# Optimization experiments

Measured on AMD Instinct MI355X. Metric: run time of the kernel, lower is better.

Reference implementation:

```python
import jax, jax.numpy as jnp
import numpy as np

THRESHOLD = 0.5        # correspondence distance threshold (init kwarg)
MAX_ITERS = 50         # fixed iteration count (open3d's max_iteration)
EPS = 1e-6


def setup_inputs() -> dict:
    key = jax.random.key(0)
    k1, k2 = jax.random.split(key)
    B, N, M = 8, 2048, 2048
    source = jax.random.normal(k1, (B, N, 3), dtype=jnp.float32)
    target = jax.random.normal(k2, (B, M, 3), dtype=jnp.float32)
    return {"source": source, "target": target}


def _icp(source, target):
    """Batched point-to-point ICP. source: (B,N,3), target: (B,M,3) -> (B,4,4)."""
    B, N, _ = source.shape
    dt = source.dtype
    t_sq = jnp.sum(target * target, axis=-1)  # (B,M), constant across iterations

    def step(T, _):
        R, tr = T[:, :3, :3], T[:, :3, 3]
        src = jnp.einsum('bij,bnj->bni', R, source) + tr[:, None, :]  # (B,N,3)
        # brute-force nearest neighbor: squared distances (B,N,M)
        d2 = (jnp.sum(src * src, axis=-1)[:, :, None]
              - 2.0 * jnp.einsum('bnd,bmd->bnm', src, target)
              + t_sq[:, None, :])
        idx = jnp.argmin(d2, axis=-1)                                   # (B,N)
        mind2 = jnp.take_along_axis(d2, idx[..., None], axis=-1)[..., 0]
        nn = jnp.take_along_axis(target, idx[..., None], axis=1)        # (B,N,3)
        # inlier mask: correspondences within threshold
        w = (mind2 < THRESHOLD * THRESHOLD).astype(dt)                  # (B,N)
        wsum = jnp.maximum(jnp.sum(w, axis=-1, keepdims=True), EPS)     # (B,1)
        cs = jnp.sum(w[..., None] * src, axis=1) / wsum                 # (B,3)
        ct = jnp.sum(w[..., None] * nn, axis=1) / wsum                  # (B,3)
        Sc = src - cs[:, None, :]
        Tc = nn - ct[:, None, :]
        # cross-covariance H = sum_n w_n (s_n - cs)(t_n - ct)^T  -> (B,3,3)
        H = jnp.einsum('bn,bni,bnj->bij', w, Sc, Tc)
        U, _, Vh = jnp.linalg.svd(H, full_matrices=False)
        V = jnp.swapaxes(Vh, -1, -2)
        # reflection fix (Kabsch): R = V diag(1,1,sign(det(V U^T))) U^T
        d = jnp.sign(jnp.linalg.det(jnp.einsum('bij,bkj->bik', V, U)))
        scale = jnp.stack([jnp.ones_like(d), jnp.ones_like(d), d], axis=-1)
        Rd = jnp.einsum('bij,bj,bkj->bik', V, scale, U)                 # (B,3,3)
        td = ct - jnp.einsum('bij,bj->bi', Rd, cs)                      # (B,3)
        top = jnp.concatenate([Rd, td[:, :, None]], axis=-1)            # (B,3,4)
        bot = jnp.broadcast_to(jnp.array([0., 0., 0., 1.], dtype=dt), (B, 1, 4))
        delta = jnp.concatenate([top, bot], axis=1)                     # (B,4,4)
        return jnp.einsum('bij,bjk->bik', delta, T), None

    T0 = jnp.broadcast_to(jnp.eye(4, dtype=dt), (B, 4, 4))
    Tfin, _ = jax.lax.scan(step, T0, None, length=MAX_ITERS)
    return Tfin


def reference(source, target):
    return _icp(source, target)
```

## Files before the change

### kernel.cpp

```cpp
#include <hip/hip_runtime.h>
#include <stdint.h>

#define BATCH 8
#define NPTS 2048
#define MPTS 2048
#define ITERS 50
#define THR2 0.25f
#define CHUNKS 32
#define SRC_PER_BLOCK 64
#define PTS 8
#define NTHREADS 1024
#define NWAVES 16
#define SLICE_LEN 16

__global__ __launch_bounds__(NTHREADS)
void icp_kernel(const float* __restrict__ src,
                const float* __restrict__ tgt,
                float* __restrict__ out,
                float* __restrict__ ws)
{
    const int tid   = threadIdx.x;
    const int blk   = blockIdx.x;
    const int b     = blk >> 5;
    const int chunk = blk & 31;
    const int g     = tid & 7;
    const int s     = tid >> 3;
    const int lane  = tid & 63;
    const int wv    = tid >> 6;

    __shared__ float4 tgt4[MPTS];
    __shared__ float  red[NWAVES][65];
    __shared__ float  srcP[SRC_PER_BLOCK][3];
    __shared__ float4 bcastT4[3];

    const float* tb = tgt + (size_t)b * MPTS * 3;
    for (int m = tid; m < MPTS; m += NTHREADS) {
        float tx = tb[m*3+0], ty = tb[m*3+1], tz = tb[m*3+2];
        tgt4[m] = make_float4(-2.f*tx, -2.f*ty, -2.f*tz, tx*tx + ty*ty + tz*tz);
    }
    const float* sb = src + (size_t)b * NPTS * 3 + (size_t)chunk * SRC_PER_BLOCK * 3;
    if (tid < SRC_PER_BLOCK) {
        srcP[tid][0] = sb[tid*3+0];
        srcP[tid][1] = sb[tid*3+1];
        srcP[tid][2] = sb[tid*3+2];
    }
    float px[PTS], py[PTS], pz[PTS];
#pragma unroll
    for (int r = 0; r < PTS; ++r) {
        int i = g*PTS + r;
        px[r] = sb[i*3+0]; py[r] = sb[i*3+1]; pz[r] = sb[i*3+2];
    }
    __syncthreads();

    float r00=1.f,r01=0.f,r02=0.f, r10=0.f,r11=1.f,r12=0.f, r20=0.f,r21=0.f,r22=1.f;
    float t0=0.f,t1=0.f,t2=0.f;

    unsigned int* bar = (unsigned int*)ws;
    float* slots = ws + 256;

    for (int it = 0; it < ITERS; ++it) {
        float sx[PTS], sy[PTS], sz[PTS];
#pragma unroll
        for (int r = 0; r < PTS; ++r) {
            sx[r] = r00*px[r] + r01*py[r] + r02*pz[r] + t0;
            sy[r] = r10*px[r] + r11*py[r] + r12*pz[r] + t1;
            sz[r] = r20*px[r] + r21*py[r] + r22*pz[r] + t2;
        }
        float best[PTS];
#pragma unroll
        for (int r = 0; r < PTS; ++r) best[r] = __int_as_float(0x7F800000);

        const int base = s * SLICE_LEN;
#pragma unroll 8
        for (int i = 0; i < SLICE_LEN; ++i) {
            int jo = (i + s) & (SLICE_LEN - 1);
            int jj = base + jo;
            float4 q = tgt4[jj];
#pragma unroll
            for (int r = 0; r < PTS; ++r) {
                float d = fmaf(sx[r], q.x, fmaf(sy[r], q.y, fmaf(sz[r], q.z, q.w)));
                unsigned int pd = (__float_as_uint(d) & 0xFFFFF800u) | (unsigned int)jj;
                best[r] = fminf(best[r], __uint_as_float(pd));
            }
        }
#pragma unroll
        for (int r = 0; r < PTS; ++r) {
            float v = best[r];
            v = fminf(v, __shfl_xor(v, 8, 64));
            v = fminf(v, __shfl_xor(v, 16, 64));
            v = fminf(v, __shfl_xor(v, 32, 64));
            best[r] = v;
        }
        if (lane < 8) {
#pragma unroll
            for (int r = 0; r < PTS; ++r) red[wv][lane*PTS + r] = best[r];
        }
        __syncthreads();

        if (tid < 64) {
            float m = red[0][tid];
#pragma unroll
            for (int ww = 1; ww < NWAVES; ++ww) m = fminf(m, red[ww][tid]);
            unsigned int mb = __float_as_uint(m);
            int   bi   = (int)(mb & 0x7FFu);
            float dmin = __uint_as_float(mb & 0xFFFFF800u);

            float ppx = srcP[tid][0], ppy = srcP[tid][1], ppz = srcP[tid][2];
            float qx = r00*ppx + r01*ppy + r02*ppz + t0;
            float qy = r10*ppx + r11*ppy + r12*ppz + t1;
            float qz = r20*ppx + r21*ppy + r22*ppz + t2;
            float s2 = qx*qx + qy*qy + qz*qz;
            float w = (dmin + s2 < THR2) ? 1.f : 0.f;
            float4 nnq = tgt4[bi];
            float nx = -0.5f*nnq.x, ny = -0.5f*nnq.y, nz = -0.5f*nnq.z;

            float v[16];
            v[0]=w;      v[1]=w*qx;    v[2]=w*qy;    v[3]=w*qz;
            v[4]=w*nx;   v[5]=w*ny;    v[6]=w*nz;
            v[7]=w*qx*nx;  v[8]=w*qx*ny;  v[9]=w*qx*nz;
            v[10]=w*qy*nx; v[11]=w*qy*ny; v[12]=w*qy*nz;
            v[13]=w*qz*nx; v[14]=w*qz*ny; v[15]=w*qz*nz;
#pragma unroll
            for (int j = 0; j < 16; ++j) {
                float a = v[j];
#pragma unroll
                for (int off = 1; off < 64; off <<= 1) a += __shfl_xor(a, off, 64);
                v[j] = a;
            }
            if (tid == 0) {
                float* sp = slots + (((size_t)(it & 1) * BATCH + b) * CHUNKS + chunk) * 16;
#pragma unroll
                for (int j = 0; j < 16; ++j)
                    __hip_atomic_store(&sp[j], v[j], __ATOMIC_RELAXED, __HIP_MEMORY_SCOPE_AGENT);
                asm volatile("s_waitcnt vmcnt(0)" ::: "memory");
                __hip_atomic_fetch_add(&bar[b*16], 1u, __ATOMIC_RELAXED, __HIP_MEMORY_SCOPE_AGENT);
                unsigned int target = (unsigned int)(CHUNKS * (it + 1));
                while (__hip_atomic_load(&bar[b*16], __ATOMIC_ACQUIRE, __HIP_MEMORY_SCOPE_AGENT) < target) {
                    __builtin_amdgcn_s_sleep(1);
                }
            }
            float S_own = 0.f;
            if (tid < 16) {
                const float* gp = slots + (((size_t)(it & 1) * BATCH + b) * CHUNKS) * 16 + tid;
                float lv[CHUNKS];
#pragma unroll
                for (int c = 0; c < CHUNKS; ++c)
                    lv[c] = __hip_atomic_load(&gp[c*16], __ATOMIC_RELAXED, __HIP_MEMORY_SCOPE_AGENT);
#pragma unroll
                for (int c = 0; c < CHUNKS; ++c) S_own += lv[c];
            }
            float S[16];
#pragma unroll
            for (int j = 0; j < 16; ++j) S[j] = __shfl(S_own, j, 64);

            float wsum = fmaxf(S[0], 1e-6f);
            float inv  = 1.f / wsum;
            float ax=S[1], ay=S[2], az=S[3], bx=S[4], by=S[5], bz=S[6];
            float H00=S[7] -ax*bx*inv, H01=S[8] -ax*by*inv, H02=S[9] -ax*bz*inv;
            float H10=S[10]-ay*bx*inv, H11=S[11]-ay*by*inv, H12=S[12]-ay*bz*inv;
            float H20=S[13]-az*bx*inv, H21=S[14]-az*by*inv, H22=S[15]-az*bz*inv;

            float a00 = H00*H00 + H10*H10 + H20*H20;
            float a01 = H00*H01 + H10*H11 + H20*H21;
            float a02 = H00*H02 + H10*H12 + H20*H22;
            float a11 = H01*H01 + H11*H11 + H21*H21;
            float a12 = H01*H02 + H11*H12 + H21*H22;
            float a22 = H02*H02 + H12*H12 + H22*H22;

            float v00=1.f,v01=0.f,v02=0.f, v10=0.f,v11=1.f,v12=0.f, v20=0.f,v21=0.f,v22=1.f;

            auto rot = [](float &app, float &aqq, float &apq,
                          float &arp, float &arq,
                          float &vp0, float &vq0, float &vp1, float &vq1, float &vp2, float &vq2) {
                float q = apq;
                if (fabsf(q) > 1e-20f) {
                    float tau = (aqq - app) / (2.f * q);
                    float tt  = (tau >= 0.f ? 1.f : -1.f) / (fabsf(tau) + sqrtf(1.f + tau*tau));
                    float c   = 1.f / sqrtf(1.f + tt*tt);
                    float sn  = tt * c;
                    app -= tt * q;
                    aqq += tt * q;
                    apq = 0.f;
                    float x = arp, y = arq;
                    arp = c*x - sn*y;  arq = sn*x + c*y;
                    float u, w2;
                    u = vp0; w2 = vq0; vp0 = c*u - sn*w2; vq0 = sn*u + c*w2;
                    u = vp1; w2 = vq1; vp1 = c*u - sn*w2; vq1 = sn*u + c*w2;
                    u = vp2; w2 = vq2; vp2 = c*u - sn*w2; vq2 = sn*u + c*w2;
                }
            };
#pragma unroll
            for (int sw = 0; sw < 5; ++sw) {
                rot(a00, a11, a01, a02, a12, v00, v01, v10, v11, v20, v21);
                rot(a00, a22, a02, a01, a12, v00, v02, v10, v12, v20, v22);
                rot(a11, a22, a12, a01, a02, v01, v02, v11, v12, v21, v22);
            }
            {
                float tmp;
                if (a00 < a11) { tmp=a00;a00=a11;a11=tmp; tmp=v00;v00=v01;v01=tmp; tmp=v10;v10=v11;v11=tmp; tmp=v20;v20=v21;v21=tmp; }
                if (a00 < a22) { tmp=a00;a00=a22;a22=tmp; tmp=v00;v00=v02;v02=tmp; tmp=v10;v10=v12;v12=tmp; tmp=v20;v20=v22;v22=tmp; }
                if (a11 < a22) { tmp=a11;a11=a22;a22=tmp; tmp=v01;v01=v02;v02=tmp; tmp=v11;v11=v12;v12=tmp; tmp=v21;v21=v22;v22=tmp; }
            }

            float Rd00=1.f,Rd01=0.f,Rd02=0.f, Rd10=0.f,Rd11=1.f,Rd12=0.f, Rd20=0.f,Rd21=0.f,Rd22=1.f;
            {
                float u0x = H00*v00 + H01*v10 + H02*v20;
                float u0y = H10*v00 + H11*v10 + H12*v20;
                float u0z = H20*v00 + H21*v10 + H22*v20;
                float n0 = sqrtf(u0x*u0x + u0y*u0y + u0z*u0z);
                if (n0 > 1e-20f) {
                    float in0 = 1.f/n0; u0x*=in0; u0y*=in0; u0z*=in0;
                    float u1x = H00*v01 + H01*v11 + H02*v21;
                    float u1y = H10*v01 + H11*v11 + H12*v21;
                    float u1z = H20*v01 + H21*v11 + H22*v21;
                    float d01 = u0x*u1x + u0y*u1y + u0z*u1z;
                    u1x -= d01*u0x; u1y -= d01*u0y; u1z -= d01*u0z;
                    float n1 = sqrtf(u1x*u1x + u1y*u1y + u1z*u1z);
                    if (!(n1 > 1e-20f)) {
                        float fx = fabsf(u0x), fy = fabsf(u0y), fz = fabsf(u0z);
                        float ex=0.f, ey=0.f, ez=0.f;
                        if (fx <= fy && fx <= fz) ex = 1.f; else if (fy <= fz) ey = 1.f; else ez = 1.f;
                        u1x = u0y*ez - u0z*ey; u1y = u0z*ex - u0x*ez; u1z = u0x*ey - u0y*ex;
                        n1 = sqrtf(u1x*u1x + u1y*u1y + u1z*u1z);
                    }
                    float in1 = 1.f/n1; u1x*=in1; u1y*=in1; u1z*=in1;
                    float u2x = u0y*u1z - u0z*u1y;
                    float u2y = u0z*u1x - u0x*u1z;
                    float u2z = u0x*u1y - u0y*u1x;
                    float detV = v00*(v11*v22 - v12*v21) - v01*(v10*v22 - v12*v20) + v02*(v10*v21 - v11*v20);
                    float dsg = (detV >= 0.f) ? 1.f : -1.f;
                    Rd00 = v00*u0x + v01*u1x + dsg*v02*u2x;
                    Rd01 = v00*u0y + v01*u1y + dsg*v02*u2y;
                    Rd02 = v00*u0z + v01*u1z + dsg*v02*u2z;
                    Rd10 = v10*u0x + v11*u1x + dsg*v12*u2x;
                    Rd11 = v10*u0y + v11*u1y + dsg*v12*u2y;
                    Rd12 = v10*u0z + v11*u1z + dsg*v12*u2z;
                    Rd20 = v20*u0x + v21*u1x + dsg*v22*u2x;
                    Rd21 = v20*u0y + v21*u1y + dsg*v22*u2y;
                    Rd22 = v20*u0z + v21*u1z + dsg*v22*u2z;
                }
            }
            float csx = ax*inv, csy = ay*inv, csz = az*inv;
            float ctx = bx*inv, cty = by*inv, ctz = bz*inv;
            float tdx = ctx - (Rd00*csx + Rd01*csy + Rd02*csz);
            float tdy = cty - (Rd10*csx + Rd11*csy + Rd12*csz);
            float tdz = ctz - (Rd20*csx + Rd21*csy + Rd22*csz);

            float nr00 = Rd00*r00 + Rd01*r10 + Rd02*r20;
            float nr01 = Rd00*r01 + Rd01*r11 + Rd02*r21;
            float nr02 = Rd00*r02 + Rd01*r12 + Rd02*r22;
            float nr10 = Rd10*r00 + Rd11*r10 + Rd12*r20;
            float nr11 = Rd10*r01 + Rd11*r11 + Rd12*r21;
            float nr12 = Rd10*r02 + Rd11*r12 + Rd12*r22;
            float nr20 = Rd20*r00 + Rd21*r10 + Rd22*r20;
            float nr21 = Rd20*r01 + Rd21*r11 + Rd22*r21;
            float nr22 = Rd20*r02 + Rd21*r12 + Rd22*r22;
            float nt0 = Rd00*t0 + Rd01*t1 + Rd02*t2 + tdx;
            float nt1 = Rd10*t0 + Rd11*t1 + Rd12*t2 + tdy;
            float nt2 = Rd20*t0 + Rd21*t1 + Rd22*t2 + tdz;

            if (tid == 0) {
                bcastT4[0] = make_float4(nr00, nr01, nr02, nt0);
                bcastT4[1] = make_float4(nr10, nr11, nr12, nt1);
                bcastT4[2] = make_float4(nr20, nr21, nr22, nt2);
            }
        }
        __syncthreads();
        float4 tA = bcastT4[0], tB = bcastT4[1], tC = bcastT4[2];
        r00=tA.x; r01=tA.y; r02=tA.z; t0=tA.w;
        r10=tB.x; r11=tB.y; r12=tB.z; t1=tB.w;
        r20=tC.x; r21=tC.y; r22=tC.z; t2=tC.w;
    }

    if (chunk == 0 && tid == 0) {
        float* o = out + (size_t)b * 16;
        o[0]=r00;  o[1]=r01;  o[2]=r02;  o[3]=t0;
        o[4]=r10;  o[5]=r11;  o[6]=r12;  o[7]=t1;
        o[8]=r20;  o[9]=r21;  o[10]=r22; o[11]=t2;
        o[12]=0.f; o[13]=0.f; o[14]=0.f; o[15]=1.f;
    }
}

extern "C" void kernel_launch(void* const* d_in, const int* in_sizes, int n_in,
                              void* d_out, int out_size, void* d_ws, size_t ws_size,
                              hipStream_t stream) {
    const float* src = (const float*)d_in[0];
    const float* tgt = (const float*)d_in[1];
    float* out = (float*)d_out;
    float* ws  = (float*)d_ws;

    hipMemsetAsync(d_ws, 0, 1024, stream);

    void* args[] = { (void*)&src, (void*)&tgt, (void*)&out, (void*)&ws };
    hipLaunchCooperativeKernel((const void*)icp_kernel,
                               dim3(BATCH * CHUNKS), dim3(NTHREADS),
                               args, 0, stream);
}
```

Before: 632.7 us.

## Spread moment reduction across whole block and interleave batch-to-block mapping

Block indices now map batch as the fast index, so blocks of different batches are interleaved across CUs. The argmin cross-lane shuffle tree is shortened to one step, with more partial rows written to shared memory (64 rows instead of 16) and reduced by the first wave. The 16-value moment reduction, previously done by one wave with 16×6 shuffles, is now an outer product spread over all 1024 threads with a shared-memory two-stage reduction. This adds extra __syncthreads barriers and a longer serial 64-row min loop in exchange for fewer serialized shuffles.

```diff
diff --git a/kernel.cpp b/kernel.cpp
--- a/kernel.cpp
+++ b/kernel.cpp
@@ -21,16 +21,19 @@
 {
     const int tid   = threadIdx.x;
     const int blk   = blockIdx.x;
-    const int b     = blk >> 5;
-    const int chunk = blk & 31;
+    const int b     = blk & 7;
+    const int chunk = blk >> 3;
     const int g     = tid & 7;
     const int s     = tid >> 3;
     const int lane  = tid & 63;
     const int wv    = tid >> 6;
 
     __shared__ float4 tgt4[MPTS];
-    __shared__ float  red[NWAVES][65];
+    __shared__ float  red[64][65];
     __shared__ float  srcP[SRC_PER_BLOCK][3];
+    __shared__ float  pf[64][4];
+    __shared__ float  pg[64][4];
+    __shared__ float  red2[16][18];
     __shared__ float4 bcastT4[3];
 
     const float* tb = tgt + (size_t)b * MPTS * 3;
@@ -86,21 +89,19 @@
 #pragma unroll
         for (int r = 0; r < PTS; ++r) {
             float v = best[r];
-            v = fminf(v, __shfl_xor(v, 8, 64));
-            v = fminf(v, __shfl_xor(v, 16, 64));
-            v = fminf(v, __shfl_xor(v, 32, 64));
-            best[r] = v;
-        }
-        if (lane < 8) {
-#pragma unroll
-            for (int r = 0; r < PTS; ++r) red[wv][lane*PTS + r] = best[r];
+            best[r] = fminf(v, __shfl_xor(v, 8, 64));
+        }
+        if ((s & 1) == 0) {
+            int row = s >> 1;
+#pragma unroll
+            for (int r = 0; r < PTS; ++r) red[row][g*PTS + r] = best[r];
         }
         __syncthreads();
 
         if (tid < 64) {
             float m = red[0][tid];
 #pragma unroll
-            for (int ww = 1; ww < NWAVES; ++ww) m = fminf(m, red[ww][tid]);
+            for (int row = 1; row < 64; ++row) m = fminf(m, red[row][tid]);
             unsigned int mb = __float_as_uint(m);
             int   bi   = (int)(mb & 0x7FFu);
             float dmin = __uint_as_float(mb & 0xFFFFF800u);
@@ -114,24 +115,31 @@
             float4 nnq = tgt4[bi];
             float nx = -0.5f*nnq.x, ny = -0.5f*nnq.y, nz = -0.5f*nnq.z;
 
-            float v[16];
-            v[0]=w;      v[1]=w*qx;    v[2]=w*qy;    v[3]=w*qz;
-            v[4]=w*nx;   v[5]=w*ny;    v[6]=w*nz;
-            v[7]=w*qx*nx;  v[8]=w*qx*ny;  v[9]=w*qx*nz;
-            v[10]=w*qy*nx; v[11]=w*qy*ny; v[12]=w*qy*nz;
-            v[13]=w*qz*nx; v[14]=w*qz*ny; v[15]=w*qz*nz;
-#pragma unroll
-            for (int j = 0; j < 16; ++j) {
-                float a = v[j];
-#pragma unroll
-                for (int off = 1; off < 64; off <<= 1) a += __shfl_xor(a, off, 64);
-                v[j] = a;
-            }
+            pf[tid][0] = w;      pf[tid][1] = w*qx;  pf[tid][2] = w*qy;  pf[tid][3] = w*qz;
+            pg[tid][0] = 1.f;    pg[tid][1] = nx;    pg[tid][2] = ny;    pg[tid][3] = nz;
+        }
+        __syncthreads();
+
+        {
+            int p = tid >> 4, c = tid & 15;
+            float v = pf[p][c >> 2] * pg[p][c & 3];
+            v += __shfl_xor(v, 16, 64);
+            v += __shfl_xor(v, 32, 64);
+            if (lane < 16) red2[wv][lane] = v;
+        }
+        __syncthreads();
+
+        if (tid < 64) {
+            int rbase = (lane >> 4) * 4;
+            int c = lane & 15;
+            float acc = ((red2[rbase+0][c] + red2[rbase+1][c]) + red2[rbase+2][c]) + red2[rbase+3][c];
+            acc += __shfl_xor(acc, 16, 64);
+            acc += __shfl_xor(acc, 32, 64);
+
+            float* sp = slots + (((size_t)(it & 1) * BATCH + b) * CHUNKS + chunk) * 16;
+            if (lane < 16)
+                __hip_atomic_store(&sp[lane], acc, __ATOMIC_RELAXED, __HIP_MEMORY_SCOPE_AGENT);
             if (tid == 0) {
-                float* sp = slots + (((size_t)(it & 1) * BATCH + b) * CHUNKS + chunk) * 16;
-#pragma unroll
-                for (int j = 0; j < 16; ++j)
-                    __hip_atomic_store(&sp[j], v[j], __ATOMIC_RELAXED, __HIP_MEMORY_SCOPE_AGENT);
                 asm volatile("s_waitcnt vmcnt(0)" ::: "memory");
                 __hip_atomic_fetch_add(&bar[b*16], 1u, __ATOMIC_RELAXED, __HIP_MEMORY_SCOPE_AGENT);
                 unsigned int target = (unsigned int)(CHUNKS * (it + 1));
@@ -144,10 +152,10 @@
                 const float* gp = slots + (((size_t)(it & 1) * BATCH + b) * CHUNKS) * 16 + tid;
                 float lv[CHUNKS];
 #pragma unroll
-                for (int c = 0; c < CHUNKS; ++c)
-                    lv[c] = __hip_atomic_load(&gp[c*16], __ATOMIC_RELAXED, __HIP_MEMORY_SCOPE_AGENT);
-#pragma unroll
-                for (int c = 0; c < CHUNKS; ++c) S_own += lv[c];
+                for (int cc = 0; cc < CHUNKS; ++cc)
+                    lv[cc] = __hip_atomic_load(&gp[cc*16], __ATOMIC_RELAXED, __HIP_MEMORY_SCOPE_AGENT);
+#pragma unroll
+                for (int cc = 0; cc < CHUNKS; ++cc) S_own += lv[cc];
             }
             float S[16];
 #pragma unroll
@@ -155,9 +163,9 @@
 
             float wsum = fmaxf(S[0], 1e-6f);
             float inv  = 1.f / wsum;
-            float ax=S[1], ay=S[2], az=S[3], bx=S[4], by=S[5], bz=S[6];
-            float H00=S[7] -ax*bx*inv, H01=S[8] -ax*by*inv, H02=S[9] -ax*bz*inv;
-            float H10=S[10]-ay*bx*inv, H11=S[11]-ay*by*inv, H12=S[12]-ay*bz*inv;
+            float ax=S[4], ay=S[8], az=S[12], bx=S[1], by=S[2], bz=S[3];
+            float H00=S[5] -ax*bx*inv, H01=S[6] -ax*by*inv, H02=S[7] -ax*bz*inv;
+            float H10=S[9] -ay*bx*inv, H11=S[10]-ay*by*inv, H12=S[11]-ay*bz*inv;
             float H20=S[13]-az*bx*inv, H21=S[14]-az*by*inv, H22=S[15]-az*bz*inv;
 
             float a00 = H00*H00 + H10*H10 + H20*H20;
```

New measurement: 672.4 us. +6.3%, slower.
